# Performance work log

Hardware: AMD Instinct MI355X
Metric: run time of the kernel (lower is better)

## Reference

```python
import jax, jax.numpy as jnp
import numpy as np

STOCH, DETER, HID, OBS, ACT = 32, 512, 512, 18, 4
MIN_STD, EPS, UPD_BIAS = 0.1, 1e-3, -1.0


def _ln(x, g, b):
    m = x.mean(-1, keepdims=True)
    v = ((x - m) ** 2).mean(-1, keepdims=True)
    return (x - m) * jax.lax.rsqrt(v + EPS) * g + b


def setup_inputs() -> dict:
    key = jax.random.key(0)
    ks = jax.random.split(key, 10)
    B, T = 256, 256
    def w(k, i, o):
        return jax.random.normal(k, (i, o), jnp.float32) / np.float32(np.sqrt(i))
    return {
        "obs": jax.random.normal(ks[0], (B, T, OBS), jnp.float32),
        "action": jax.random.normal(ks[1], (B, T, ACT), jnp.float32),
        "is_first": jax.random.randint(ks[2], (B, T), 0, 2, jnp.int32),
        "w_prior_in": w(ks[3], STOCH + ACT, HID),
        "g_prior_in": jnp.ones(HID, jnp.float32),
        "bb_prior_in": jnp.zeros(HID, jnp.float32),
        "w_gru": w(ks[4], HID + DETER, 3 * DETER),
        "g_gru": jnp.ones(3 * DETER, jnp.float32),
        "bb_gru": jnp.zeros(3 * DETER, jnp.float32),
        "w_prior_out": w(ks[5], DETER, HID),
        "g_prior_out": jnp.ones(HID, jnp.float32),
        "bb_prior_out": jnp.zeros(HID, jnp.float32),
        "w_prior_stats": w(ks[6], HID, 2 * STOCH),
        "b_prior_stats": jnp.zeros(2 * STOCH, jnp.float32),
        "w_post": w(ks[7], DETER + OBS, HID),
        "g_post": jnp.ones(HID, jnp.float32),
        "bb_post": jnp.zeros(HID, jnp.float32),
        "w_post_stats": w(ks[8], HID, 2 * STOCH),
        "b_post_stats": jnp.zeros(2 * STOCH, jnp.float32),
        "initial_deter": 0.1 * jax.random.normal(ks[9], (1, DETER), jnp.float32),
    }


def reference(obs, action, is_first,
              w_prior_in, g_prior_in, bb_prior_in,
              w_gru, g_gru, bb_gru,
              w_prior_out, g_prior_out, bb_prior_out,
              w_prior_stats, b_prior_stats,
              w_post, g_post, bb_post,
              w_post_stats, b_post_stats,
              initial_deter):
    """RSSM.observe with sample=False. Returns (B, T, 2*(DETER+3*STOCH)):
    concat of post[deter,stoch,mean,std] and prior[deter,stoch,mean,std];
    stoch == mean since dist.mean is used."""
    B = obs.shape[0]
    # learned initial state (identical for every batch row / reset)
    deter0 = jnp.tanh(initial_deter)                                  # (1, DETER)
    h0 = jax.nn.silu(_ln(deter0 @ w_prior_out, g_prior_out, bb_prior_out))
    s0 = h0 @ w_prior_stats + b_prior_stats
    init_mean, _ = jnp.split(s0, 2, axis=-1)                          # (1, STOCH)

    def step(carry, xs):
        deter, stoch = carry
        o_t, a_t, f_t = xs
        mask = (f_t > 0)[:, None]
        deter = jnp.where(mask, deter0, deter)
        stoch = jnp.where(mask, init_mean, stoch)
        a_t = jnp.where(mask, 0.0, a_t)
        # prior_in
        h = jax.nn.silu(_ln(jnp.concatenate([stoch, a_t], -1) @ w_prior_in,
                            g_prior_in, bb_prior_in))
        # GRU cell (depth=1)
        gates = _ln(jnp.concatenate([h, deter], -1) @ w_gru, g_gru, bb_gru)
        r, c, u = jnp.split(gates, 3, axis=-1)
        r = jax.nn.sigmoid(r)
        u = jax.nn.sigmoid(u + UPD_BIAS)
        cand = jax.nn.silu(r * c)
        deter = u * cand + (1.0 - u) * deter
        # prior stats
        h2 = jax.nn.silu(_ln(deter @ w_prior_out, g_prior_out, bb_prior_out))
        ps = h2 @ w_prior_stats + b_prior_stats
        pm, psd = jnp.split(ps, 2, axis=-1)
        psd = jax.nn.softplus(psd) + MIN_STD
        # posterior
        h3 = jax.nn.silu(_ln(jnp.concatenate([deter, o_t], -1) @ w_post,
                             g_post, bb_post))
        qs = h3 @ w_post_stats + b_post_stats
        qm, qsd = jnp.split(qs, 2, axis=-1)
        qsd = jax.nn.softplus(qsd) + MIN_STD
        out = jnp.concatenate([deter, qm, qm, qsd, deter, pm, pm, psd], -1)
        return (deter, qm), out

    carry0 = (jnp.broadcast_to(deter0, (B, DETER)),
              jnp.broadcast_to(init_mean, (B, STOCH)))
    xs = (obs.swapaxes(0, 1), action.swapaxes(0, 1), is_first.swapaxes(0, 1))
    _, ys = jax.lax.scan(step, carry0, xs)   # (T, B, 2*(DETER+3*STOCH))
    return ys.swapaxes(0, 1)
```

## Files before the change

### kernel.cpp

```cpp
#include <hip/hip_runtime.h>

#define TT 256
#define BDIM 256

typedef unsigned short u16;
typedef unsigned int u32;
typedef __attribute__((ext_vector_type(8))) short bf16x8;
typedef __attribute__((ext_vector_type(4))) float f32x4;

#define GLL(g, l) __builtin_amdgcn_global_load_lds( \
    (const __attribute__((address_space(1))) void*)(g), \
    (__attribute__((address_space(3))) void*)(l), 16, 0, 0)

struct P {
  const float* obs; const float* action; const int* is_first;
  const float* w_prior_in; const float* g_prior_in; const float* bb_prior_in;
  const float* w_gru; const float* g_gru; const float* bb_gru;
  const float* w_prior_out; const float* g_prior_out; const float* bb_prior_out;
  const float* w_prior_stats; const float* b_prior_stats;
  const float* w_post; const float* g_post; const float* bb_post;
  const float* w_post_stats; const float* b_post_stats;
  const float* initial_deter;
  float* out;
  u16 *WgT3;
  u16 *W2T3;
  u16 *WsT3;
  float *wpiT;
  float *deter0, *init_mean;
  int *segb, *segt0, *nact;
  u16 *h2;
  int NB;
};

__device__ __forceinline__ float b2f(u16 u) {
  union { float f; u32 i; } v; v.i = ((u32)u) << 16; return v.f;
}
__device__ __forceinline__ u16 f2b(float f) {
  union { float f; u32 i; } v; v.f = f;
  u32 r = v.i + 0x7FFF + ((v.i >> 16) & 1);
  return (u16)(r >> 16);
}
__device__ __forceinline__ float sigm(float x) { return 1.f / (1.f + __expf(-x)); }
__device__ __forceinline__ float splus(float x) { return x > 15.f ? x : log1pf(__expf(x)); }

__device__ __forceinline__ void awr2(u16* base, int i, int kk, u16 hi, u16 lo) {
  int o = (kk >> 5) << 11;
  int sw = ((i << 5) + (kk & 31)) ^ ((i & 7) << 3);
  base[o + sw] = hi;
  base[o + 1024 + sw] = lo;
}

__device__ __forceinline__ void h_from_x(const P& p, u16* arow, int i, float xv, int lane) {
  float xs[36];
  #pragma unroll
  for (int j = 0; j < 36; ++j) xs[j] = __shfl(xv, j, 64);
  float a0[8];
  #pragma unroll
  for (int c = 0; c < 8; ++c) {
    const float4* wp = (const float4*)(p.wpiT + (size_t)(lane + (c << 6)) * 36);
    float s = 0.f;
    #pragma unroll
    for (int t4 = 0; t4 < 9; ++t4) {
      float4 ww = wp[t4];
      s = fmaf(xs[4 * t4], ww.x, s); s = fmaf(xs[4 * t4 + 1], ww.y, s);
      s = fmaf(xs[4 * t4 + 2], ww.z, s); s = fmaf(xs[4 * t4 + 3], ww.w, s);
    }
    a0[c] = s;
  }
  float sm = 0.f, sq = 0.f;
  #pragma unroll
  for (int c = 0; c < 8; ++c) { sm += a0[c]; sq += a0[c] * a0[c]; }
  #pragma unroll
  for (int o = 32; o; o >>= 1) { sm += __shfl_xor(sm, o); sq += __shfl_xor(sq, o); }
  float m = sm * (1.f / 512.f);
  float rs = rsqrtf(sq * (1.f / 512.f) - m * m + 1e-3f);
  #pragma unroll
  for (int c = 0; c < 8; ++c) {
    int col = lane + (c << 6);
    float v = (a0[c] - m) * rs * p.g_prior_in[col] + p.bb_prior_in[col];
    v = v * sigm(v);
    u16 hi = f2b(v);
    awr2(arow, i, 544 + col, hi, f2b(v - b2f(hi)));
  }
}

__global__ void k_weights(P p) {
  const int E1 = 1024 * 1536, E2 = 544 * 1024, E3 = 1024 * 128, E4 = 36 * 512;
  const int total = E1 + E2 + E3 + E4;
  for (int idx = blockIdx.x * blockDim.x + threadIdx.x; idx < total;
       idx += gridDim.x * blockDim.x) {
    if (idx < E1) {
      int k = idx / 1536, n = idx - k * 1536;
      float w = (k < 512) ? p.w_gru[(512 + k) * 1536 + n] : p.w_gru[(k - 512) * 1536 + n];
      int np = n >> 8, r = n & 255, pc = k >> 5, kk = k & 31;
      u16* d = p.WgT3 + ((size_t)(pc * 6 + np) << 14) + (r << 5) + kk;
      u16 hi = f2b(w); d[0] = hi; d[8192] = f2b(w - b2f(hi));
    } else if (idx < E1 + E2) {
      int t = idx - E1; int k = t >> 10, n = t & 1023;
      float w;
      if (k < 512) w = (n < 512) ? p.w_prior_out[k * 512 + n] : p.w_post[k * 512 + (n - 512)];
      else { int j = k - 512; w = (n >= 512 && j < 18) ? p.w_post[(512 + j) * 512 + (n - 512)] : 0.f; }
      int np = n >> 8, r = n & 255, pc = k >> 5, kk = k & 31;
      u16* d = p.W2T3 + ((size_t)(pc * 4 + np) << 14) + (r << 5) + kk;
      u16 hi = f2b(w); d[0] = hi; d[8192] = f2b(w - b2f(hi));
    } else if (idx < E1 + E2 + E3) {
      int t = idx - E1 - E2; int k = t >> 7, n = t & 127;
      float w;
      if (n < 64) w = (k < 512) ? p.w_prior_stats[k * 64 + n] : 0.f;
      else        w = (k >= 512) ? p.w_post_stats[(k - 512) * 64 + (n - 64)] : 0.f;
      int pc = k >> 5, kk = k & 31;
      u16* d = p.WsT3 + ((size_t)pc << 13) + (n << 5) + kk;
      u16 hi = f2b(w); d[0] = hi; d[4096] = f2b(w - b2f(hi));
    } else {
      int t = idx - E1 - E2 - E3; int j = t >> 9, col = t & 511;
      p.wpiT[col * 36 + j] = p.w_prior_in[j * 512 + col];
    }
  }
}

__global__ void k_init_state(P p) {
  __shared__ float d0s[512], tmp[512], red[256];
  int tid = threadIdx.x;
  for (int n = tid; n < 512; n += 256) { d0s[n] = tanhf(p.initial_deter[n]); p.deter0[n] = d0s[n]; }
  __syncthreads();
  for (int n = tid; n < 512; n += 256) {
    float s = 0.f;
    for (int d = 0; d < 512; ++d) s = fmaf(d0s[d], p.w_prior_out[d * 512 + n], s);
    tmp[n] = s;
  }
  __syncthreads();
  float ls = 0.f, lq = 0.f;
  for (int n = tid; n < 512; n += 256) { ls += tmp[n]; lq += tmp[n] * tmp[n]; }
  red[tid] = ls; __syncthreads();
  for (int s = 128; s; s >>= 1) { if (tid < s) red[tid] += red[tid + s]; __syncthreads(); }
  float m = red[0] * (1.f / 512.f); __syncthreads();
  red[tid] = lq; __syncthreads();
  for (int s = 128; s; s >>= 1) { if (tid < s) red[tid] += red[tid + s]; __syncthreads(); }
  float rs = rsqrtf(red[0] * (1.f / 512.f) - m * m + 1e-3f); __syncthreads();
  for (int n = tid; n < 512; n += 256) {
    float h = (tmp[n] - m) * rs * p.g_prior_out[n] + p.bb_prior_out[n];
    tmp[n] = h * sigm(h);
  }
  __syncthreads();
  if (tid < 32) {
    float s = 0.f;
    for (int d = 0; d < 512; ++d) s = fmaf(tmp[d], p.w_prior_stats[d * 64 + tid], s);
    p.init_mean[tid] = s + p.b_prior_stats[tid];
  }
}

__global__ void k_segments(P p) {
  __shared__ int hist[257], off[258], cur[257];
  int tid = threadIdx.x;
  for (int i = tid; i < 257; i += 256) hist[i] = 0;
  __syncthreads();
  int b = tid;
  { int t = 0;
    while (t < TT) {
      int t0 = t; t++;
      while (t < TT && p.is_first[b * TT + t] == 0) t++;
      atomicAdd(&hist[t - t0], 1);
    } }
  __syncthreads();
  if (tid == 0) {
    int run = 0;
    for (int len = 256; len >= 0; --len) { off[len] = run; run += hist[len]; }
  }
  __syncthreads();
  for (int i = tid; i < 257; i += 256) { cur[i] = off[i]; p.nact[i] = off[i]; }
  __syncthreads();
  { int t = 0;
    while (t < TT) {
      int t0 = t; t++;
      while (t < TT && p.is_first[b * TT + t] == 0) t++;
      int idx = atomicAdd(&cur[t - t0], 1);
      p.segb[idx] = b; p.segt0[idx] = t0;
    } }
}

template<int NSTEPS, int JAT>
__device__ __forceinline__ void gemm_nb(
    const u16* aLds, const u16* wImg, size_t wStride,
    int wave, int quad, int l15, int xr, f32x4 (&acc)[2][4]) {
  const u16* wq = wImg + ((((wave << 6) + l15) << 5) + (quad << 3));
  bf16x8 H0[4], L0[4], H1[4], L1[4], H2[4], L2[4];
  auto ld = [&](bf16x8 (&H)[4], bf16x8 (&L)[4]) {
    #pragma unroll
    for (int ni = 0; ni < 4; ++ni) {
      H[ni] = *(const bf16x8*)(wq + (ni << 9));
      L[ni] = *(const bf16x8*)(wq + 8192 + (ni << 9));
    }
    wq += wStride;
  };
  auto cp = [&](int st, bf16x8 (&H)[4], bf16x8 (&L)[4]) {
    int apc = st + (st >= JAT ? 1 : 0);
    const u16* A = aLds + (apc << 11);
    bf16x8 ah[2], al[2];
    #pragma unroll
    for (int mi = 0; mi < 2; ++mi) {
      int off = ((((mi << 4) + l15) << 5) + (quad << 3)) ^ xr;
      ah[mi] = *(const bf16x8*)&A[off];
      al[mi] = *(const bf16x8*)&A[off + 1024];
    }
    #pragma unroll
    for (int ni = 0; ni < 4; ++ni)
      #pragma unroll
      for (int mi = 0; mi < 2; ++mi) {
        acc[mi][ni] = __builtin_amdgcn_mfma_f32_16x16x32_bf16(ah[mi], H[ni], acc[mi][ni], 0, 0, 0);
        acc[mi][ni] = __builtin_amdgcn_mfma_f32_16x16x32_bf16(al[mi], H[ni], acc[mi][ni], 0, 0, 0);
        acc[mi][ni] = __builtin_amdgcn_mfma_f32_16x16x32_bf16(ah[mi], L[ni], acc[mi][ni], 0, 0, 0);
      }
  };
  static_assert(NSTEPS % 3 == 2, "tail assumes NSTEPS==2 mod 3");
  ld(H0, L0); ld(H1, L1);
  for (int st = 0; st + 2 < NSTEPS; st += 3) {
    ld(H2, L2); cp(st, H0, L0);
    ld(H0, L0); cp(st + 1, H1, L1);
    ld(H1, L1); cp(st + 2, H2, L2);
  }
  cp(NSTEPS - 2, H0, L0);
  cp(NSTEPS - 1, H1, L1);
}

__global__ void __launch_bounds__(BDIM, 1) k_main(P p) {
  __shared__ u16 lds[73728];
  __shared__ float lnscr[4][32][4];
  __shared__ float stochs[1024];
  __shared__ int orowt[32];
  const int tid = threadIdx.x;
  const int wave = tid >> 6, lane = tid & 63, quad = lane >> 4, l15 = lane & 15;
  const int xr = (l15 & 7) << 3;
  u16* arow = lds;
  u16* fb = lds + 67584;
  const int blk = blockIdx.x;
  u16* slotH = p.h2 + (size_t)blk * 65536;
  const int S_total = p.nact[0];
  const int ntiles = (S_total + 31) >> 5;
  const int gmax = (ntiles + 255) & ~255;

  for (int g = blk; g < gmax; g += p.NB) {
    int rr_ = g >> 8, w = g & 255;
    int x = w & 7; if (rr_ & 1) x = 7 - x;
    int t = (rr_ << 8) + (x << 5) + ((w >> 3) & 31);
    if (t >= ntiles) continue;
    int row0 = t << 5;
    int nr0 = S_total - row0; if (nr0 > 32) nr0 = 32;

    for (int k = 0;; ++k) {
      int Mk = p.nact[k] - row0; if (Mk > nr0) Mk = nr0;
      if (Mk <= 0) break;

      if (tid < 32)
        orowt[tid] = (tid < Mk) ? (p.segb[row0 + tid] * TT + p.segt0[row0 + tid] + k) : -1;
      for (int i = wave; i < Mk; i += 4) {
        int gi = row0 + i;
        int b = p.segb[gi], t0 = p.segt0[gi];
        float xv = 0.f;
        if (k == 0) {
          #pragma unroll
          for (int c = 0; c < 8; ++c) {
            int d = lane + (c << 6);
            float v = p.deter0[d];
            u16 hi = f2b(v);
            awr2(arow, i, d, hi, f2b(v - b2f(hi)));
          }
          int ff = p.is_first[b * TT + t0];
          if (lane < 32) xv = p.init_mean[lane];
          else if (lane < 36) xv = (ff > 0) ? 0.f : p.action[((size_t)b * TT + t0) * 4 + (lane - 32)];
        } else {
          if (lane < 32) xv = stochs[(i << 5) + lane];
          else if (lane < 36) xv = p.action[((size_t)b * TT + t0 + k) * 4 + (lane - 32)];
        }
        int tc = t0 + k;
        if (lane < 32) {
          float ov = (lane < 18) ? p.obs[((size_t)b * TT + tc) * 18 + lane] : 0.f;
          u16 hi = f2b(ov);
          awr2(arow, i, 512 + lane, hi, f2b(ov - b2f(hi)));
        }
        h_from_x(p, arow, i, xv, lane);
      }
      __syncthreads();

      f32x4 acc[6][2][4];
      #pragma unroll
      for (int np = 0; np < 6; ++np) {
        #pragma unroll
        for (int mi = 0; mi < 2; ++mi)
          #pragma unroll
          for (int ni = 0; ni < 4; ++ni) acc[np][mi][ni] = f32x4{0.f, 0.f, 0.f, 0.f};
        gemm_nb<32, 16>(arow, p.WgT3 + np * 16384, (size_t)6 * 16384,
                        wave, quad, l15, xr, acc[np]);
      }
      __syncthreads();

      {
        float smv[2][4], sqv[2][4];
        #pragma unroll
        for (int mi = 0; mi < 2; ++mi)
          #pragma unroll
          for (int rg = 0; rg < 4; ++rg) { smv[mi][rg] = 0.f; sqv[mi][rg] = 0.f; }
        #pragma unroll
        for (int np = 0; np < 6; ++np)
          #pragma unroll
          for (int mi = 0; mi < 2; ++mi)
            #pragma unroll
            for (int ni = 0; ni < 4; ++ni)
              #pragma unroll
              for (int rg = 0; rg < 4; ++rg) {
                float v = acc[np][mi][ni][rg];
                smv[mi][rg] += v; sqv[mi][rg] += v * v;
              }
        #pragma unroll
        for (int mi = 0; mi < 2; ++mi)
          #pragma unroll
          for (int rg = 0; rg < 4; ++rg) {
            float s = smv[mi][rg], qv = sqv[mi][rg];
            #pragma unroll
            for (int o = 1; o < 16; o <<= 1) { s += __shfl_xor(s, o); qv += __shfl_xor(qv, o); }
            smv[mi][rg] = s; sqv[mi][rg] = qv;
          }
        if (l15 == 0) {
          #pragma unroll
          for (int mi = 0; mi < 2; ++mi)
            #pragma unroll
            for (int rg = 0; rg < 4; ++rg) {
              int row = (mi << 4) + (quad << 2) + rg;
              lnscr[wave][row][0] = smv[mi][rg];
              lnscr[wave][row][1] = sqv[mi][rg];
            }
        }
        __syncthreads();
        #pragma unroll
        for (int mi = 0; mi < 2; ++mi)
          #pragma unroll
          for (int rg = 0; rg < 4; ++rg) {
            int row = (mi << 4) + (quad << 2) + rg;
            float a0 = 0.f, a1 = 0.f;
            #pragma unroll
            for (int w2 = 0; w2 < 4; ++w2) {
              a0 += lnscr[w2][row][0]; a1 += lnscr[w2][row][1];
            }
            float m_ = a0 * (1.f / 1536.f);
            smv[mi][rg] = m_;
            sqv[mi][rg] = rsqrtf(a1 * (1.f / 1536.f) - m_ * m_ + 1e-3f);
          }
        #pragma unroll
        for (int hh = 0; hh < 2; ++hh)
          #pragma unroll
          for (int ni = 0; ni < 4; ++ni) {
            int dcol = (hh << 8) + (wave << 6) + (ni << 4) + l15;
            float gR = p.g_gru[dcol], gC = p.g_gru[512 + dcol], gU = p.g_gru[1024 + dcol];
            float bR = p.bb_gru[dcol], bC = p.bb_gru[512 + dcol], bU = p.bb_gru[1024 + dcol];
            int pcD = dcol >> 5, kkD = dcol & 31;
            #pragma unroll
            for (int mi = 0; mi < 2; ++mi)
              #pragma unroll
              for (int rg = 0; rg < 4; ++rg) {
                int row = (mi << 4) + (quad << 2) + rg;
                float m_ = smv[mi][rg], rs_ = sqv[mi][rg];
                float vr = (acc[hh][mi][ni][rg] - m_) * rs_ * gR + bR;
                float vc = (acc[2 + hh][mi][ni][rg] - m_) * rs_ * gC + bC;
                float vu = (acc[4 + hh][mi][ni][rg] - m_) * rs_ * gU + bU;
                float r_ = sigm(vr), u_ = sigm(vu - 1.f);
                float rc = r_ * vc, cand = rc * sigm(rc);
                int ab = (pcD << 11) + (((row << 5) + kkD) ^ ((row & 7) << 3));
                float dp = b2f(arow[ab]) + b2f(arow[ab + 1024]);
                float dn = u_ * cand + (1.f - u_) * dp;
                u16 hi = f2b(dn);
                arow[ab] = hi; arow[ab + 1024] = f2b(dn - b2f(hi));
                int ot = orowt[row];
                if (ot >= 0) {
                  float* orow = p.out + (size_t)ot * 1216;
                  orow[dcol] = dn; orow[608 + dcol] = dn;
                }
              }
          }
      }
      __syncthreads();

      f32x4 dac[4][2][4];
      #pragma unroll
      for (int np = 0; np < 4; ++np) {
        #pragma unroll
        for (int mi = 0; mi < 2; ++mi)
          #pragma unroll
          for (int ni = 0; ni < 4; ++ni) dac[np][mi][ni] = f32x4{0.f, 0.f, 0.f, 0.f};
        gemm_nb<17, 100>(arow, p.W2T3 + np * 16384, (size_t)4 * 16384,
                         wave, quad, l15, xr, dac[np]);
      }
      {
        float sP[2][4], qP[2][4], sQ[2][4], qQ[2][4];
        #pragma unroll
        for (int mi = 0; mi < 2; ++mi)
          #pragma unroll
          for (int rg = 0; rg < 4; ++rg) { sP[mi][rg]=0.f; qP[mi][rg]=0.f; sQ[mi][rg]=0.f; qQ[mi][rg]=0.f; }
        #pragma unroll
        for (int np = 0; np < 4; ++np)
          #pragma unroll
          for (int mi = 0; mi < 2; ++mi)
            #pragma unroll
            for (int ni = 0; ni < 4; ++ni)
              #pragma unroll
              for (int rg = 0; rg < 4; ++rg) {
                float v = dac[np][mi][ni][rg];
                if (np < 2) { sP[mi][rg] += v; qP[mi][rg] += v * v; }
                else        { sQ[mi][rg] += v; qQ[mi][rg] += v * v; }
              }
        #pragma unroll
        for (int mi = 0; mi < 2; ++mi)
          #pragma unroll
          for (int rg = 0; rg < 4; ++rg) {
            float a0 = sP[mi][rg], a1 = qP[mi][rg], a2 = sQ[mi][rg], a3 = qQ[mi][rg];
            #pragma unroll
            for (int o = 1; o < 16; o <<= 1) {
              a0 += __shfl_xor(a0, o); a1 += __shfl_xor(a1, o);
              a2 += __shfl_xor(a2, o); a3 += __shfl_xor(a3, o);
            }
            sP[mi][rg] = a0; qP[mi][rg] = a1; sQ[mi][rg] = a2; qQ[mi][rg] = a3;
          }
        if (l15 == 0) {
          #pragma unroll
          for (int mi = 0; mi < 2; ++mi)
            #pragma unroll
            for (int rg = 0; rg < 4; ++rg) {
              int row = (mi << 4) + (quad << 2) + rg;
              lnscr[wave][row][0] = sP[mi][rg]; lnscr[wave][row][1] = qP[mi][rg];
              lnscr[wave][row][2] = sQ[mi][rg]; lnscr[wave][row][3] = qQ[mi][rg];
            }
        }
        __syncthreads();
        float mP[2][4], rP[2][4], mQ[2][4], rQ[2][4];
        #pragma unroll
        for (int mi = 0; mi < 2; ++mi)
          #pragma unroll
          for (int rg = 0; rg < 4; ++rg) {
            int row = (mi << 4) + (quad << 2) + rg;
            float a0 = 0.f, a1 = 0.f, a2 = 0.f, a3 = 0.f;
            #pragma unroll
            for (int w2 = 0; w2 < 4; ++w2) {
              a0 += lnscr[w2][row][0]; a1 += lnscr[w2][row][1];
              a2 += lnscr[w2][row][2]; a3 += lnscr[w2][row][3];
            }
            mP[mi][rg] = a0 * (1.f / 512.f);
            rP[mi][rg] = rsqrtf(a1 * (1.f / 512.f) - mP[mi][rg] * mP[mi][rg] + 1e-3f);
            mQ[mi][rg] = a2 * (1.f / 512.f);
            rQ[mi][rg] = rsqrtf(a3 * (1.f / 512.f) - mQ[mi][rg] * mQ[mi][rg] + 1e-3f);
          }
        #pragma unroll
        for (int np = 0; np < 4; ++np) {
          const int half = np >> 1;
          #pragma unroll
          for (int ni = 0; ni < 4; ++ni) {
            int col = (np << 8) + (wave << 6) + (ni << 4) + l15;
            int c5 = col & 511;
            float gv = half ? p.g_post[c5] : p.g_prior_out[c5];
            float bv = half ? p.bb_post[c5] : p.bb_prior_out[c5];
            int pcH = col >> 5, kkH = col & 31;
            #pragma unroll
            for (int mi = 0; mi < 2; ++mi)
              #pragma unroll
              for (int rg = 0; rg < 4; ++rg) {
                int row = (mi << 4) + (quad << 2) + rg;
                float m_ = half ? mQ[mi][rg] : mP[mi][rg];
                float rs_ = half ? rQ[mi][rg] : rP[mi][rg];
                float xx = (dac[np][mi][ni][rg] - m_) * rs_ * gv + bv;
                xx = xx * sigm(xx);
                u16 hi = f2b(xx);
                size_t e = ((size_t)pcH << 11) + (((row << 5) + kkH) ^ ((row & 7) << 3));
                slotH[e] = hi; slotH[e + 1024] = f2b(xx - b2f(hi));
              }
          }
        }
      }
      __syncthreads();

      {
        const u16* wq0 = p.WsT3 + (((wave << 5) + l15) << 5) + (quad << 3);
        f32x4 fac[2][2];
        #pragma unroll
        for (int mi = 0; mi < 2; ++mi)
          #pragma unroll
          for (int ni = 0; ni < 2; ++ni) fac[mi][ni] = f32x4{0.f, 0.f, 0.f, 0.f};
        bf16x8 FH0[2], FL0[2], FH1[2], FL1[2];
        auto stF = [&](int st, int buf) {
          GLL(slotH + (st << 11) + (wave << 9) + (lane << 3),
              fb + (buf << 11) + (wave << 9));
        };
        auto ldF = [&](int st, bf16x8 (&FH)[2], bf16x8 (&FL)[2]) {
          const u16* qq = wq0 + ((size_t)st << 13);
          #pragma unroll
          for (int ni = 0; ni < 2; ++ni) {
            FH[ni] = *(const bf16x8*)(qq + (ni << 9));
            FL[ni] = *(const bf16x8*)(qq + 4096 + (ni << 9));
          }
        };
        auto cpF = [&](int st, bf16x8 (&FH)[2], bf16x8 (&FL)[2]) {
          const u16* A = fb + ((st % 3) << 11);
          bf16x8 ah[2], al[2];
          #pragma unroll
          for (int mi = 0; mi < 2; ++mi) {
            int off = ((((mi << 4) + l15) << 5) + (quad << 3)) ^ xr;
            ah[mi] = *(const bf16x8*)&A[off];
            al[mi] = *(const bf16x8*)&A[off + 1024];
          }
          #pragma unroll
          for (int ni = 0; ni < 2; ++ni)
            #pragma unroll
            for (int mi = 0; mi < 2; ++mi) {
              fac[mi][ni] = __builtin_amdgcn_mfma_f32_16x16x32_bf16(ah[mi], FH[ni], fac[mi][ni], 0, 0, 0);
              fac[mi][ni] = __builtin_amdgcn_mfma_f32_16x16x32_bf16(al[mi], FH[ni], fac[mi][ni], 0, 0, 0);
              fac[mi][ni] = __builtin_amdgcn_mfma_f32_16x16x32_bf16(ah[mi], FL[ni], fac[mi][ni], 0, 0, 0);
            }
        };
        stF(0, 0); stF(1, 1); ldF(0, FH0, FL0);
        for (int st = 0; st < 32; st += 2) {
          asm volatile("s_waitcnt vmcnt(5)" ::: "memory");
          __builtin_amdgcn_s_barrier();
          __builtin_amdgcn_sched_barrier(0);
          if (st + 2 < 32) stF(st + 2, (st + 2) % 3);
          ldF(st + 1, FH1, FL1);
          cpF(st, FH0, FL0);
          asm volatile("s_waitcnt vmcnt(5)" ::: "memory");
          __builtin_amdgcn_s_barrier();
          __builtin_amdgcn_sched_barrier(0);
          if (st + 3 < 32) stF(st + 3, (st + 3) % 3);
          if (st + 2 < 32) ldF(st + 2, FH0, FL0);
          cpF(st + 1, FH1, FL1);
        }
        #pragma unroll
        for (int mi = 0; mi < 2; ++mi)
          #pragma unroll
          for (int ni = 0; ni < 2; ++ni)
            #pragma unroll
            for (int rg = 0; rg < 4; ++rg) {
              int i = (mi << 4) + (quad << 2) + rg;
              int col = (wave << 5) + (ni << 4) + l15;
              if (i < Mk) {
                float v = fac[mi][ni][rg];
                int ot = orowt[i];
                float* orow = p.out + (size_t)ot * 1216;
                if (col < 32) {
                  v += p.b_prior_stats[col];
                  orow[1120 + col] = v; orow[1152 + col] = v;
                } else if (col < 64) {
                  v = splus(v + p.b_prior_stats[col]) + 0.1f;
                  orow[1184 + col - 32] = v;
                } else if (col < 96) {
                  v += p.b_post_stats[col - 64];
                  orow[512 + col - 64] = v; orow[544 + col - 64] = v;
                  stochs[(i << 5) + (col - 64)] = v;
                } else {
                  v = splus(v + p.b_post_stats[col - 64]) + 0.1f;
                  orow[576 + col - 96] = v;
                }
              }
            }
      }
      __syncthreads();
    }
  }
}

extern "C" void kernel_launch(void* const* d_in, const int* in_sizes, int n_in,
                              void* d_out, int out_size, void* d_ws, size_t ws_size,
                              hipStream_t stream) {
  P p;
  p.obs = (const float*)d_in[0];
  p.action = (const float*)d_in[1];
  p.is_first = (const int*)d_in[2];
  p.w_prior_in = (const float*)d_in[3];
  p.g_prior_in = (const float*)d_in[4];
  p.bb_prior_in = (const float*)d_in[5];
  p.w_gru = (const float*)d_in[6];
  p.g_gru = (const float*)d_in[7];
  p.bb_gru = (const float*)d_in[8];
  p.w_prior_out = (const float*)d_in[9];
  p.g_prior_out = (const float*)d_in[10];
  p.bb_prior_out = (const float*)d_in[11];
  p.w_prior_stats = (const float*)d_in[12];
  p.b_prior_stats = (const float*)d_in[13];
  p.w_post = (const float*)d_in[14];
  p.g_post = (const float*)d_in[15];
  p.bb_post = (const float*)d_in[16];
  p.w_post_stats = (const float*)d_in[17];
  p.b_post_stats = (const float*)d_in[18];
  p.initial_deter = (const float*)d_in[19];
  p.out = (float*)d_out;

  char* w = (char*)d_ws;
  auto alloc = [&](size_t bytes) -> char* {
    char* r = w; w += (bytes + 255) & ~(size_t)255; return r;
  };
  p.WgT3 = (u16*)alloc((size_t)192 * 16384 * 2);
  p.W2T3 = (u16*)alloc((size_t)68 * 16384 * 2);
  p.WsT3 = (u16*)alloc((size_t)32 * 8192 * 2);
  p.wpiT = (float*)alloc((size_t)512 * 36 * 4);
  p.deter0 = (float*)alloc(512 * 4);
  p.init_mean = (float*)alloc(32 * 4);
  p.segb = (int*)alloc((size_t)65536 * 4);
  p.segt0 = (int*)alloc((size_t)65536 * 4);
  p.nact = (int*)alloc(257 * 4);
  size_t used = (size_t)(w - (char*)d_ws);
  size_t avail = ws_size > used ? ws_size - used : 0;
  long long nb = (long long)(avail / 131072);
  if (nb > 256) nb = 256;
  if (nb < 1) nb = 1;
  p.NB = (int)nb;
  p.h2 = (u16*)alloc((size_t)p.NB * 131072);

  k_weights<<<dim3(256), dim3(256), 0, stream>>>(p);
  k_init_state<<<dim3(1), dim3(256), 0, stream>>>(p);
  k_segments<<<dim3(1), dim3(256), 0, stream>>>(p);
  k_main<<<dim3(p.NB), dim3(BDIM), 0, stream>>>(p);
}
```

Measured before the change: 9.857 ms.

## Double block to 8 waves, keep h2 in LDS, single-bf16 stats GEMM

Raises the workgroup from 4 to 8 waves so each wave computes half as many output columns per GEMM, and rewrites the weight-prefetch pipeline as a 4-slot ring. The post-LayerNorm hidden activations now stay in LDS as a single bf16 value instead of going through a per-block global scratch with hi/lo split and global_load_lds staging. The final stats GEMM therefore drops the low-part MFMA on the activations. This removes global round trips and barriers but lowers precision on the stats path and fixes the grid at 256 blocks.

```diff
diff --git a/kernel.cpp b/kernel.cpp
--- a/kernel.cpp
+++ b/kernel.cpp
@@ -1,16 +1,13 @@
 #include <hip/hip_runtime.h>
 
 #define TT 256
-#define BDIM 256
+#define BDIM 512
+#define GRID 256
 
 typedef unsigned short u16;
 typedef unsigned int u32;
 typedef __attribute__((ext_vector_type(8))) short bf16x8;
 typedef __attribute__((ext_vector_type(4))) float f32x4;
-
-#define GLL(g, l) __builtin_amdgcn_global_load_lds( \
-    (const __attribute__((address_space(1))) void*)(g), \
-    (__attribute__((address_space(3))) void*)(l), 16, 0, 0)
 
 struct P {
   const float* obs; const float* action; const int* is_first;
@@ -28,8 +25,6 @@
   float *wpiT;
   float *deter0, *init_mean;
   int *segb, *segt0, *nact;
-  u16 *h2;
-  int NB;
 };
 
 __device__ __forceinline__ float b2f(u16 u) {
@@ -178,21 +173,21 @@
     } }
 }
 
-template<int NSTEPS, int JAT>
+template<int NI, int NSTEPS, int JAT>
 __device__ __forceinline__ void gemm_nb(
-    const u16* aLds, const u16* wImg, size_t wStride,
-    int wave, int quad, int l15, int xr, f32x4 (&acc)[2][4]) {
-  const u16* wq = wImg + ((((wave << 6) + l15) << 5) + (quad << 3));
-  bf16x8 H0[4], L0[4], H1[4], L1[4], H2[4], L2[4];
-  auto ld = [&](bf16x8 (&H)[4], bf16x8 (&L)[4]) {
+    const u16* aLds, const u16* __restrict__ wBase, int wStrideU16,
+    int wave, int quad, int l15, int xr, f32x4 (&acc)[2][NI]) {
+  const u16* wq = wBase + (((wave * (NI * 16) + l15) << 5) + (quad << 3));
+  bf16x8 H[4][NI], L[4][NI];
+  auto ld = [&](int st, int s) {
+    const u16* q = wq + (size_t)st * wStrideU16;
     #pragma unroll
-    for (int ni = 0; ni < 4; ++ni) {
-      H[ni] = *(const bf16x8*)(wq + (ni << 9));
-      L[ni] = *(const bf16x8*)(wq + 8192 + (ni << 9));
+    for (int ni = 0; ni < NI; ++ni) {
+      H[s][ni] = *(const bf16x8*)(q + (ni << 9));
+      L[s][ni] = *(const bf16x8*)(q + 8192 + (ni << 9));
     }
-    wq += wStride;
   };
-  auto cp = [&](int st, bf16x8 (&H)[4], bf16x8 (&L)[4]) {
+  auto cp = [&](int st, int s) {
     int apc = st + (st >= JAT ? 1 : 0);
     const u16* A = aLds + (apc << 11);
     bf16x8 ah[2], al[2];
@@ -203,42 +198,37 @@
       al[mi] = *(const bf16x8*)&A[off + 1024];
     }
     #pragma unroll
-    for (int ni = 0; ni < 4; ++ni)
+    for (int ni = 0; ni < NI; ++ni)
       #pragma unroll
       for (int mi = 0; mi < 2; ++mi) {
-        acc[mi][ni] = __builtin_amdgcn_mfma_f32_16x16x32_bf16(ah[mi], H[ni], acc[mi][ni], 0, 0, 0);
-        acc[mi][ni] = __builtin_amdgcn_mfma_f32_16x16x32_bf16(al[mi], H[ni], acc[mi][ni], 0, 0, 0);
-        acc[mi][ni] = __builtin_amdgcn_mfma_f32_16x16x32_bf16(ah[mi], L[ni], acc[mi][ni], 0, 0, 0);
+        acc[mi][ni] = __builtin_amdgcn_mfma_f32_16x16x32_bf16(ah[mi], H[s][ni], acc[mi][ni], 0, 0, 0);
+        acc[mi][ni] = __builtin_amdgcn_mfma_f32_16x16x32_bf16(al[mi], H[s][ni], acc[mi][ni], 0, 0, 0);
+        acc[mi][ni] = __builtin_amdgcn_mfma_f32_16x16x32_bf16(ah[mi], L[s][ni], acc[mi][ni], 0, 0, 0);
       }
   };
-  static_assert(NSTEPS % 3 == 2, "tail assumes NSTEPS==2 mod 3");
-  ld(H0, L0); ld(H1, L1);
-  for (int st = 0; st + 2 < NSTEPS; st += 3) {
-    ld(H2, L2); cp(st, H0, L0);
-    ld(H0, L0); cp(st + 1, H1, L1);
-    ld(H1, L1); cp(st + 2, H2, L2);
-  }
-  cp(NSTEPS - 2, H0, L0);
-  cp(NSTEPS - 1, H1, L1);
+  ld(0, 0); ld(1, 1); ld(2, 2);
+  #pragma unroll
+  for (int st = 0; st < NSTEPS; ++st) {
+    if (st + 3 < NSTEPS) ld(st + 3, (st + 3) & 3);
+    cp(st, st & 3);
+  }
 }
 
 __global__ void __launch_bounds__(BDIM, 1) k_main(P p) {
-  __shared__ u16 lds[73728];
-  __shared__ float lnscr[4][32][4];
+  __shared__ u16 arow[67584];
+  __shared__ float lnscr[8][32][4];
   __shared__ float stochs[1024];
   __shared__ int orowt[32];
   const int tid = threadIdx.x;
   const int wave = tid >> 6, lane = tid & 63, quad = lane >> 4, l15 = lane & 15;
   const int xr = (l15 & 7) << 3;
-  u16* arow = lds;
-  u16* fb = lds + 67584;
+  u16* h2l = arow + 34816;
   const int blk = blockIdx.x;
-  u16* slotH = p.h2 + (size_t)blk * 65536;
   const int S_total = p.nact[0];
   const int ntiles = (S_total + 31) >> 5;
   const int gmax = (ntiles + 255) & ~255;
 
-  for (int g = blk; g < gmax; g += p.NB) {
+  for (int g = blk; g < gmax; g += GRID) {
     int rr_ = g >> 8, w = g & 255;
     int x = w & 7; if (rr_ & 1) x = 7 - x;
     int t = (rr_ << 8) + (x << 5) + ((w >> 3) & 31);
@@ -252,7 +242,7 @@
 
       if (tid < 32)
         orowt[tid] = (tid < Mk) ? (p.segb[row0 + tid] * TT + p.segt0[row0 + tid] + k) : -1;
-      for (int i = wave; i < Mk; i += 4) {
+      for (int i = wave; i < Mk; i += 8) {
         int gi = row0 + i;
         int b = p.segb[gi], t0 = p.segt0[gi];
         float xv = 0.f;
@@ -281,15 +271,15 @@
       }
       __syncthreads();
 
-      f32x4 acc[6][2][4];
+      f32x4 acc[6][2][2];
       #pragma unroll
       for (int np = 0; np < 6; ++np) {
         #pragma unroll
         for (int mi = 0; mi < 2; ++mi)
           #pragma unroll
-          for (int ni = 0; ni < 4; ++ni) acc[np][mi][ni] = f32x4{0.f, 0.f, 0.f, 0.f};
-        gemm_nb<32, 16>(arow, p.WgT3 + np * 16384, (size_t)6 * 16384,
-                        wave, quad, l15, xr, acc[np]);
+          for (int ni = 0; ni < 2; ++ni) acc[np][mi][ni] = f32x4{0.f, 0.f, 0.f, 0.f};
+        gemm_nb<2, 32, 16>(arow, p.WgT3 + np * 16384, 6 * 16384,
+                           wave, quad, l15, xr, acc[np]);
       }
       __syncthreads();
 
@@ -304,7 +294,7 @@
           #pragma unroll
           for (int mi = 0; mi < 2; ++mi)
             #pragma unroll
-            for (int ni = 0; ni < 4; ++ni)
+            for (int ni = 0; ni < 2; ++ni)
               #pragma unroll
               for (int rg = 0; rg < 4; ++rg) {
                 float v = acc[np][mi][ni][rg];
@@ -337,9 +327,7 @@
             int row = (mi << 4) + (quad << 2) + rg;
             float a0 = 0.f, a1 = 0.f;
             #pragma unroll
-            for (int w2 = 0; w2 < 4; ++w2) {
-              a0 += lnscr[w2][row][0]; a1 += lnscr[w2][row][1];
-            }
+            for (int w2 = 0; w2 < 8; ++w2) { a0 += lnscr[w2][row][0]; a1 += lnscr[w2][row][1]; }
             float m_ = a0 * (1.f / 1536.f);
             smv[mi][rg] = m_;
             sqv[mi][rg] = rsqrtf(a1 * (1.f / 1536.f) - m_ * m_ + 1e-3f);
@@ -347,8 +335,8 @@
         #pragma unroll
         for (int hh = 0; hh < 2; ++hh)
           #pragma unroll
-          for (int ni = 0; ni < 4; ++ni) {
-            int dcol = (hh << 8) + (wave << 6) + (ni << 4) + l15;
+          for (int ni = 0; ni < 2; ++ni) {
+            int dcol = (hh << 8) + (wave << 5) + (ni << 4) + l15;
             float gR = p.g_gru[dcol], gC = p.g_gru[512 + dcol], gU = p.g_gru[1024 + dcol];
             float bR = p.bb_gru[dcol], bC = p.bb_gru[512 + dcol], bU = p.bb_gru[1024 + dcol];
             int pcD = dcol >> 5, kkD = dcol & 31;
@@ -378,16 +366,17 @@
       }
       __syncthreads();
 
-      f32x4 dac[4][2][4];
+      f32x4 dac[4][2][2];
       #pragma unroll
       for (int np = 0; np < 4; ++np) {
         #pragma unroll
         for (int mi = 0; mi < 2; ++mi)
           #pragma unroll
-          for (int ni = 0; ni < 4; ++ni) dac[np][mi][ni] = f32x4{0.f, 0.f, 0.f, 0.f};
-        gemm_nb<17, 100>(arow, p.W2T3 + np * 16384, (size_t)4 * 16384,
-                         wave, quad, l15, xr, dac[np]);
-      }
+          for (int ni = 0; ni < 2; ++ni) dac[np][mi][ni] = f32x4{0.f, 0.f, 0.f, 0.f};
+        gemm_nb<2, 17, 100>(arow, p.W2T3 + np * 16384, 4 * 16384,
+                            wave, quad, l15, xr, dac[np]);
+      }
+
       {
         float sP[2][4], qP[2][4], sQ[2][4], qQ[2][4];
         #pragma unroll
@@ -399,7 +388,7 @@
           #pragma unroll
           for (int mi = 0; mi < 2; ++mi)
             #pragma unroll
-            for (int ni = 0; ni < 4; ++ni)
+            for (int ni = 0; ni < 2; ++ni)
               #pragma unroll
               for (int rg = 0; rg < 4; ++rg) {
                 float v = dac[np][mi][ni][rg];
@@ -437,7 +426,7 @@
             int row = (mi << 4) + (quad << 2) + rg;
             float a0 = 0.f, a1 = 0.f, a2 = 0.f, a3 = 0.f;
             #pragma unroll
-            for (int w2 = 0; w2 < 4; ++w2) {
+            for (int w2 = 0; w2 < 8; ++w2) {
               a0 += lnscr[w2][row][0]; a1 += lnscr[w2][row][1];
               a2 += lnscr[w2][row][2]; a3 += lnscr[w2][row][3];
             }
@@ -450,8 +439,8 @@
         for (int np = 0; np < 4; ++np) {
           const int half = np >> 1;
           #pragma unroll
-          for (int ni = 0; ni < 4; ++ni) {
-            int col = (np << 8) + (wave << 6) + (ni << 4) + l15;
+          for (int ni = 0; ni < 2; ++ni) {
+            int col = (np << 8) + (wave << 5) + (ni << 4) + l15;
             int c5 = col & 511;
             float gv = half ? p.g_post[c5] : p.g_prior_out[c5];
             float bv = half ? p.bb_post[c5] : p.bb_prior_out[c5];
@@ -465,9 +454,7 @@
                 float rs_ = half ? rQ[mi][rg] : rP[mi][rg];
                 float xx = (dac[np][mi][ni][rg] - m_) * rs_ * gv + bv;
                 xx = xx * sigm(xx);
-                u16 hi = f2b(xx);
-                size_t e = ((size_t)pcH << 11) + (((row << 5) + kkH) ^ ((row & 7) << 3));
-                slotH[e] = hi; slotH[e + 1024] = f2b(xx - b2f(hi));
+                h2l[(pcH << 10) + (((row << 5) + kkH) ^ ((row & 7) << 3))] = f2b(xx);
               }
           }
         }
@@ -475,86 +462,58 @@
       __syncthreads();
 
       {
-        const u16* wq0 = p.WsT3 + (((wave << 5) + l15) << 5) + (quad << 3);
-        f32x4 fac[2][2];
-        #pragma unroll
-        for (int mi = 0; mi < 2; ++mi)
-          #pragma unroll
-          for (int ni = 0; ni < 2; ++ni) fac[mi][ni] = f32x4{0.f, 0.f, 0.f, 0.f};
-        bf16x8 FH0[2], FL0[2], FH1[2], FL1[2];
-        auto stF = [&](int st, int buf) {
-          GLL(slotH + (st << 11) + (wave << 9) + (lane << 3),
-              fb + (buf << 11) + (wave << 9));
+        const u16* wqF = p.WsT3 + (((wave << 4) + l15) << 5) + (quad << 3);
+        f32x4 fac[2];
+        fac[0] = f32x4{0.f, 0.f, 0.f, 0.f};
+        fac[1] = f32x4{0.f, 0.f, 0.f, 0.f};
+        bf16x8 FH[4], FL[4];
+        auto ldF = [&](int st, int s) {
+          const u16* q = wqF + (st << 13);
+          FH[s] = *(const bf16x8*)(q);
+          FL[s] = *(const bf16x8*)(q + 4096);
         };
-        auto ldF = [&](int st, bf16x8 (&FH)[2], bf16x8 (&FL)[2]) {
-          const u16* qq = wq0 + ((size_t)st << 13);
-          #pragma unroll
-          for (int ni = 0; ni < 2; ++ni) {
-            FH[ni] = *(const bf16x8*)(qq + (ni << 9));
-            FL[ni] = *(const bf16x8*)(qq + 4096 + (ni << 9));
-          }
-        };
-        auto cpF = [&](int st, bf16x8 (&FH)[2], bf16x8 (&FL)[2]) {
-          const u16* A = fb + ((st % 3) << 11);
-          bf16x8 ah[2], al[2];
+        auto cpF = [&](int st, int s) {
+          const u16* A = h2l + (st << 10);
           #pragma unroll
           for (int mi = 0; mi < 2; ++mi) {
             int off = ((((mi << 4) + l15) << 5) + (quad << 3)) ^ xr;
-            ah[mi] = *(const bf16x8*)&A[off];
-            al[mi] = *(const bf16x8*)&A[off + 1024];
-          }
-          #pragma unroll
-          for (int ni = 0; ni < 2; ++ni)
-            #pragma unroll
-            for (int mi = 0; mi < 2; ++mi) {
-              fac[mi][ni] = __builtin_amdgcn_mfma_f32_16x16x32_bf16(ah[mi], FH[ni], fac[mi][ni], 0, 0, 0);
-              fac[mi][ni] = __builtin_amdgcn_mfma_f32_16x16x32_bf16(al[mi], FH[ni], fac[mi][ni], 0, 0, 0);
-              fac[mi][ni] = __builtin_amdgcn_mfma_f32_16x16x32_bf16(ah[mi], FL[ni], fac[mi][ni], 0, 0, 0);
-            }
+            bf16x8 ah = *(const bf16x8*)&A[off];
+            fac[mi] = __builtin_amdgcn_mfma_f32_16x16x32_bf16(ah, FH[s], fac[mi], 0, 0, 0);
+            fac[mi] = __builtin_amdgcn_mfma_f32_16x16x32_bf16(ah, FL[s], fac[mi], 0, 0, 0);
+          }
         };
-        stF(0, 0); stF(1, 1); ldF(0, FH0, FL0);
-        for (int st = 0; st < 32; st += 2) {
-          asm volatile("s_waitcnt vmcnt(5)" ::: "memory");
-          __builtin_amdgcn_s_barrier();
-          __builtin_amdgcn_sched_barrier(0);
-          if (st + 2 < 32) stF(st + 2, (st + 2) % 3);
-          ldF(st + 1, FH1, FL1);
-          cpF(st, FH0, FL0);
-          asm volatile("s_waitcnt vmcnt(5)" ::: "memory");
-          __builtin_amdgcn_s_barrier();
-          __builtin_amdgcn_sched_barrier(0);
-          if (st + 3 < 32) stF(st + 3, (st + 3) % 3);
-          if (st + 2 < 32) ldF(st + 2, FH0, FL0);
-          cpF(st + 1, FH1, FL1);
+        ldF(0, 0); ldF(1, 1); ldF(2, 2);
+        #pragma unroll
+        for (int st = 0; st < 32; ++st) {
+          if (st + 3 < 32) ldF(st + 3, (st + 3) & 3);
+          cpF(st, st & 3);
         }
         #pragma unroll
         for (int mi = 0; mi < 2; ++mi)
           #pragma unroll
-          for (int ni = 0; ni < 2; ++ni)
-            #pragma unroll
-            for (int rg = 0; rg < 4; ++rg) {
-              int i = (mi << 4) + (quad << 2) + rg;
-              int col = (wave << 5) + (ni << 4) + l15;
-              if (i < Mk) {
-                float v = fac[mi][ni][rg];
-                int ot = orowt[i];
-                float* orow = p.out + (size_t)ot * 1216;
-                if (col < 32) {
-                  v += p.b_prior_stats[col];
-                  orow[1120 + col] = v; orow[1152 + col] = v;
-                } else if (col < 64) {
-                  v = splus(v + p.b_prior_stats[col]) + 0.1f;
-                  orow[1184 + col - 32] = v;
-                } else if (col < 96) {
-                  v += p.b_post_stats[col - 64];
-                  orow[512 + col - 64] = v; orow[544 + col - 64] = v;
-                  stochs[(i << 5) + (col - 64)] = v;
-                } else {
-                  v = splus(v + p.b_post_stats[col - 64]) + 0.1f;
-                  orow[576 + col - 96] = v;
-                }
+          for (int rg = 0; rg < 4; ++rg) {
+            int i = (mi << 4) + (quad << 2) + rg;
+            int col = (wave << 4) + l15;
+            if (i < Mk) {
+              float v = fac[mi][rg];
+              int ot = orowt[i];
+              float* orow = p.out + (size_t)ot * 1216;
+              if (col < 32) {
+                v += p.b_prior_stats[col];
+                orow[1120 + col] = v; orow[1152 + col] = v;
+              } else if (col < 64) {
+                v = splus(v + p.b_prior_stats[col]) + 0.1f;
+                orow[1184 + col - 32] = v;
+              } else if (col < 96) {
+                v += p.b_post_stats[col - 64];
+                orow[512 + col - 64] = v; orow[544 + col - 64] = v;
+                stochs[(i << 5) + (col - 64)] = v;
+              } else {
+                v = splus(v + p.b_post_stats[col - 64]) + 0.1f;
+                orow[576 + col - 96] = v;
               }
             }
+          }
       }
       __syncthreads();
     }
@@ -600,16 +559,9 @@
   p.segb = (int*)alloc((size_t)65536 * 4);
   p.segt0 = (int*)alloc((size_t)65536 * 4);
   p.nact = (int*)alloc(257 * 4);
-  size_t used = (size_t)(w - (char*)d_ws);
-  size_t avail = ws_size > used ? ws_size - used : 0;
-  long long nb = (long long)(avail / 131072);
-  if (nb > 256) nb = 256;
-  if (nb < 1) nb = 1;
-  p.NB = (int)nb;
-  p.h2 = (u16*)alloc((size_t)p.NB * 131072);
 
   k_weights<<<dim3(256), dim3(256), 0, stream>>>(p);
   k_init_state<<<dim3(1), dim3(256), 0, stream>>>(p);
   k_segments<<<dim3(1), dim3(256), 0, stream>>>(p);
-  k_main<<<dim3(p.NB), dim3(BDIM), 0, stream>>>(p);
-}
+  k_main<<<dim3(GRID), dim3(BDIM), 0, stream>>>(p);
+}
```

Measured after the change: 13.52 ms. 1.37x slower.
